# Kernel tuning notes

Measured on AMD Instinct MI355X. Metric: run time of the kernel, lower is better.

The kernel has to match this reference:

```python
import jax, jax.numpy as jnp
import numpy as np

C = 256
P = 8          # partition_size
DH = 32        # dim_head
NH = C // DH   # num heads
EXP = 4        # mlp expansion
EPS = 1e-5


def conv2d(x, w, b, stride, pad, groups):
    # x: NCHW, w: (O, I/groups, kh, kw)
    y = jax.lax.conv_general_dilated(
        x, w, (stride, stride), [(pad, pad), (pad, pad)],
        dimension_numbers=('NCHW', 'OIHW', 'NCHW'), feature_group_count=groups)
    return y + b[None, :, None, None]


def layernorm(x, g, b):
    m = jnp.mean(x, axis=-1, keepdims=True)
    v = jnp.mean((x - m) ** 2, axis=-1, keepdims=True)
    return (x - m) * jax.lax.rsqrt(v + EPS) * g + b


def partition_block(x):
    # (B,H,W,C) -> (B*nH*nW, P, P, C), MaxViT 'block' mode
    B, H, W, c = x.shape
    x = x.reshape(B, H // P, P, W // P, P, c)
    return x.transpose(0, 1, 3, 2, 4, 5).reshape(-1, P, P, c)


def reverse_block(w, H, W):
    c = w.shape[-1]
    x = w.reshape(-1, H // P, W // P, P, P, c)
    return x.transpose(0, 1, 3, 2, 4, 5).reshape(-1, H, W, c)


def window_attn(xw, qkv_w, qkv_b, proj_w, proj_b):
    # xw: (Nw, P, P, C); faithful to SelfAttentionCl (dropout inactive at eval)
    Nw = xw.shape[0]
    L = P * P
    qkv = xw.reshape(Nw, L, C) @ qkv_w.T + qkv_b           # (Nw, L, 3C)
    qkv = qkv.reshape(Nw, L, NH, 3 * DH).transpose(0, 2, 1, 3)  # (Nw, nh, L, 3dh)
    q, k, v = jnp.split(qkv, 3, axis=-1)
    attn = jax.nn.softmax((q @ jnp.swapaxes(k, -1, -2)) * (DH ** -0.5), axis=-1)
    o = (attn @ v).transpose(0, 2, 1, 3).reshape(Nw, P, P, C)
    return o @ proj_w.T + proj_b


def setup_inputs() -> dict:
    key = jax.random.key(0)
    ks = jax.random.split(key, 16)
    s = 0.02
    d = {
        'x': jax.random.normal(ks[0], (2, C, 256, 256), jnp.float32),
        'h': jnp.zeros((2, 256, 256, C), jnp.float32),
        'conv_w': s * jax.random.normal(ks[1], (C, 1, 3, 3), jnp.float32),
        'conv_b': jnp.zeros((C,), jnp.float32),
        'comb_w': s * jax.random.normal(ks[2], (C, 2, 7, 7), jnp.float32),
        'comb_b': jnp.zeros((C,), jnp.float32),
        'ln1_g': jnp.ones((C,), jnp.float32), 'ln1_b': jnp.zeros((C,), jnp.float32),
        'ln2_g': jnp.ones((C,), jnp.float32), 'ln2_b': jnp.zeros((C,), jnp.float32),
        'ln3_g': jnp.ones((C,), jnp.float32), 'ln3_b': jnp.zeros((C,), jnp.float32),
        'fsa_ln_g': jnp.ones((C,), jnp.float32), 'fsa_ln_b': jnp.zeros((C,), jnp.float32),
        'qkv_w': s * jax.random.normal(ks[3], (3 * C, C), jnp.float32),
        'qkv_b': jnp.zeros((3 * C,), jnp.float32),
        'proj_w': s * jax.random.normal(ks[4], (C, C), jnp.float32),
        'proj_b': jnp.zeros((C,), jnp.float32),
        'mlp_w1': s * jax.random.normal(ks[5], (EXP * C, C), jnp.float32),
        'mlp_b1': jnp.zeros((EXP * C,), jnp.float32),
        'mlp_w2': s * jax.random.normal(ks[6], (C, EXP * C), jnp.float32),
        'mlp_b2': jnp.zeros((C,), jnp.float32),
        'convg_w': s * jax.random.normal(ks[7], (C, 1, 7, 7), jnp.float32),
        'convg_b': jnp.zeros((C,), jnp.float32),
        'convh_w': s * jax.random.normal(ks[8], (C, 1, 7, 7), jnp.float32),
        'convh_b': jnp.zeros((C,), jnp.float32),
        'convf_w': s * jax.random.normal(ks[9], (C // 4, 4, 3, 3), jnp.float32),
        'convf_b': jnp.zeros((C // 4,), jnp.float32),
    }
    return d


def reference(x, h, conv_w, conv_b, comb_w, comb_b, ln1_g, ln1_b, ln2_g, ln2_b,
              ln3_g, ln3_b, fsa_ln_g, fsa_ln_b, qkv_w, qkv_b, proj_w, proj_b,
              mlp_w1, mlp_b1, mlp_w2, mlp_b2, convg_w, convg_b, convh_w, convh_b,
              convf_w, convf_b):
    relu = jax.nn.relu
    # depthwise conv + relu + LN (channels-last)
    x_conv = relu(conv2d(x, conv_w, conv_b, 1, 1, C)).transpose(0, 2, 3, 1)  # NHWC
    x_conv = layernorm(x_conv, ln1_g, ln1_b)
    H, W = x_conv.shape[1], x_conv.shape[2]
    # combine with recurrent state via grouped 7x7 conv (groups=C, 2 in-ch per group)
    xc = jnp.concatenate((x_conv, h), axis=3).transpose(0, 3, 1, 2)  # (B,2C,H,W)
    xc = conv2d(xc, comb_w, comb_b, 1, 3, C).transpose(0, 2, 3, 1)
    xc = layernorm(relu(xc), ln2_g, ln2_b)
    # block-windowed self-attention (UnifiedBlockGridAttention, mode='block')
    y = layernorm(xc, fsa_ln_g, fsa_ln_b)
    wins = partition_block(y)
    a = window_attn(wins, qkv_w, qkv_b, proj_w, proj_b)
    x_bsa = reverse_block(a, H, W)
    x_bsa = x_bsa + xc  # DropPath inactive (eval)
    x_bsa = layernorm(relu(x_bsa), ln3_g, ln3_b)
    # MLP (Linear -> GELU -> Linear), channels-last
    x_bsa = jax.nn.gelu(x_bsa @ mlp_w1.T + mlp_b1) @ mlp_w2.T + mlp_b2
    # output heads: depthwise 7x7 convs + grouped 3x3
    x_bsa = x_bsa.transpose(0, 3, 1, 2)
    x_bsa = relu(conv2d(x_bsa, convg_w, convg_b, 1, 3, C))
    h_new = relu(conv2d(x_bsa, convh_w, convh_b, 1, 3, C).transpose(0, 2, 3, 1))
    x_out = relu(conv2d(x_bsa, convf_w, convf_b, 1, 1, C // 4))
    return (x_out, h_new)
```

## Files before the change

kernel.cpp:

```cpp
#include <hip/hip_runtime.h>
#include <hip/hip_bf16.h>

#define HD 256
#define WD 256
#define CH 256
#define NB 2
#define NPIX (NB*HD*WD)

typedef __attribute__((ext_vector_type(4))) float f32x4;
typedef __attribute__((ext_vector_type(8))) short bf16x8;
typedef __attribute__((ext_vector_type(4))) short bf16x4;

__device__ __forceinline__ short f2bf(float f){
  unsigned u = __float_as_uint(f);
  u += 0x7fffu + ((u>>16)&1u);
  return (short)(u>>16);
}

__device__ __forceinline__ f32x4 mfma_bf16(bf16x8 a, bf16x8 b, f32x4 c){
  asm("v_mfma_f32_16x16x32_bf16 %0, %1, %2, %0" : "+v"(c) : "v"(a), "v"(b));
  return c;
}

__global__ __launch_bounds__(256) void k_cvtw(const float* __restrict__ qkvw,
    const float* __restrict__ projw, const float* __restrict__ w1,
    const float* __restrict__ w2, short* __restrict__ out){
  int i = blockIdx.x*256 + threadIdx.x;
  float v;
  if (i < 196608) v = qkvw[i];
  else if (i < 262144) v = projw[i-196608];
  else if (i < 524288) v = w1[i-262144];
  else v = w2[i-524288];
  out[i] = f2bf(v);
}

__global__ __launch_bounds__(256) void k_prepw(const float* __restrict__ combw,
    const float* __restrict__ gw, const float* __restrict__ hw,
    const float* __restrict__ fw, float* __restrict__ wT){
  int i = blockIdx.x*256 + threadIdx.x;
  if (i < 25088){
    int wi = i>>9, r = i&511, ii = r>>8, o = r&255;
    wT[i] = combw[o*98 + ii*49 + wi];
  } else if (i < 37632){
    int j = i-25088; int wi = j>>8, c = j&255;
    wT[i] = gw[c*49 + wi];
  } else if (i < 50176){
    int j = i-37632; int wi = j>>8, c = j&255;
    wT[i] = hw[c*49 + wi];
  } else if (i < 52480){
    int j = i-50176; int tap = j>>8, r = j&255, oc = r>>2, ic = r&3;
    wT[i] = fw[oc*36 + ic*9 + tap];
  }
}

__global__ __launch_bounds__(256) void k_conv3(const float* __restrict__ x,
    const float* __restrict__ w, const float* __restrict__ bias,
    const float* __restrict__ g1, const float* __restrict__ b1,
    float* __restrict__ out){
  int bid = blockIdx.x;
  int xb = bid & 15, y = (bid>>4) & 255, b = bid>>12;
  int t = threadIdx.x;
  __shared__ float tile[16][268];
  int xx0 = xb*16;
  {
    int xi = t & 15, cg = t >> 4;
    int xxg = xx0 + xi;
    #pragma unroll
    for (int k=0;k<16;++k){
      int c = cg*16 + k;
      const float* xp = x + ((size_t)(b*CH + c)*HD)*WD;
      float acc = bias[c];
      #pragma unroll
      for (int dy=-1; dy<=1; ++dy){
        int yy = y+dy;
        if ((unsigned)yy >= HD) continue;
        #pragma unroll
        for (int dx=-1; dx<=1; ++dx){
          int x2 = xxg+dx;
          if ((unsigned)x2 >= WD) continue;
          acc += xp[yy*WD + x2] * w[c*9 + (dy+1)*3 + (dx+1)];
        }
      }
      tile[xi][c] = fmaxf(acc, 0.f);
    }
  }
  __syncthreads();
  {
    int px = t >> 4, cs = t & 15;
    float4 m[4];
    #pragma unroll
    for (int j=0;j<4;++j) m[j] = *(const float4*)(&tile[px][cs*16 + j*4]);
    float s = 0.f, q = 0.f;
    #pragma unroll
    for (int j=0;j<4;++j){
      s += m[j].x+m[j].y+m[j].z+m[j].w;
      q += m[j].x*m[j].x+m[j].y*m[j].y+m[j].z*m[j].z+m[j].w*m[j].w;
    }
    #pragma unroll
    for (int o=1;o<16;o<<=1){ s += __shfl_xor(s,o); q += __shfl_xor(q,o); }
    float mean = s*(1.f/CH);
    float r = rsqrtf(q*(1.f/CH) - mean*mean + 1e-5f);
    size_t n = (size_t)(b*HD + y)*WD + xx0 + px;
    float* op = out + n*CH + cs*16;
    #pragma unroll
    for (int j=0;j<4;++j){
      float4 G = *(const float4*)(g1 + cs*16 + j*4);
      float4 Bb = *(const float4*)(b1 + cs*16 + j*4);
      float4 o4;
      o4.x = (m[j].x-mean)*r*G.x + Bb.x;
      o4.y = (m[j].y-mean)*r*G.y + Bb.y;
      o4.z = (m[j].z-mean)*r*G.z + Bb.z;
      o4.w = (m[j].w-mean)*r*G.w + Bb.w;
      *(float4*)(op + j*4) = o4;
    }
  }
}

__global__ __launch_bounds__(256) void k_comb(const float* __restrict__ xconv,
    const float* __restrict__ hbuf, const float* __restrict__ wT,
    const float* __restrict__ bias,
    const float* __restrict__ g2, const float* __restrict__ b2,
    const float* __restrict__ gf, const float* __restrict__ bfv,
    float* __restrict__ xc, short* __restrict__ ybuf){
  int bid = blockIdx.x;
  int xg = bid & 63, yb = (bid>>6) & 63, b = bid>>12;
  int wv = threadIdx.x>>6, lane = threadIdx.x & 63;
  int xx = xg*4 + wv, y0 = yb*4;
  const float* S = (lane < 32) ? xconv : hbuf;
  int cin = 8*(lane & 31);
  float4 bv = ((const float4*)bias)[lane];
  float4 acc[4];
  #pragma unroll
  for (int i=0;i<4;++i) acc[i] = bv;
  bool inty = (y0 >= 3) && (y0 <= HD-7);
  #pragma unroll 1
  for (int dx=0; dx<7; ++dx){
    int x2 = xx + dx - 3;
    bool vx = (unsigned)x2 < WD;
    float4 rA[10], rB[10];
    if (vx && inty){
      const float* base = S + ((size_t)((b*HD + y0-3)*WD + x2))*CH + cin;
      #pragma unroll
      for (int k=0;k<10;++k){
        const float4* p = (const float4*)(base + (size_t)k*WD*CH);
        rA[k] = p[0]; rB[k] = p[1];
      }
    } else {
      #pragma unroll
      for (int k=0;k<10;++k){
        int yy = y0 + k - 3;
        if (vx && (unsigned)yy < HD){
          const float4* p = (const float4*)(S + ((size_t)((b*HD+yy)*WD + x2))*CH + cin);
          rA[k] = p[0]; rB[k] = p[1];
        } else {
          rA[k] = float4{0,0,0,0}; rB[k] = float4{0,0,0,0};
        }
      }
    }
    #pragma unroll
    for (int dy=0; dy<7; ++dy){
      int wi = dy*7 + dx;
      float4 wa = ((const float4*)(wT + wi*512))[lane];
      float4 wb4 = ((const float4*)(wT + wi*512 + 256))[lane];
      #pragma unroll
      for (int yi=0; yi<4; ++yi){
        int k = yi + dy;
        acc[yi].x += rA[k].x*wa.x + rA[k].y*wb4.x;
        acc[yi].y += rA[k].z*wa.y + rA[k].w*wb4.y;
        acc[yi].z += rB[k].x*wa.z + rB[k].y*wb4.z;
        acc[yi].w += rB[k].z*wa.w + rB[k].w*wb4.w;
      }
    }
  }
  float4 G2 = ((const float4*)g2)[lane],  B2 = ((const float4*)b2)[lane];
  float4 GF = ((const float4*)gf)[lane],  BF = ((const float4*)bfv)[lane];
  #pragma unroll
  for (int yi=0; yi<4; ++yi){
    float4 v;
    v.x = fmaxf(acc[yi].x, 0.f); v.y = fmaxf(acc[yi].y, 0.f);
    v.z = fmaxf(acc[yi].z, 0.f); v.w = fmaxf(acc[yi].w, 0.f);
    float s = v.x+v.y+v.z+v.w;
    float q = v.x*v.x+v.y*v.y+v.z*v.z+v.w*v.w;
    #pragma unroll
    for (int o=1;o<64;o<<=1){ s += __shfl_xor(s,o); q += __shfl_xor(q,o); }
    float mean = s*(1.f/CH);
    float r = rsqrtf(q*(1.f/CH) - mean*mean + 1e-5f);
    float4 w4;
    w4.x = (v.x-mean)*r*G2.x + B2.x;
    w4.y = (v.y-mean)*r*G2.y + B2.y;
    w4.z = (v.z-mean)*r*G2.z + B2.z;
    w4.w = (v.w-mean)*r*G2.w + B2.w;
    size_t n = (size_t)((b*HD + y0+yi)*WD + xx);
    ((float4*)(xc + n*CH))[lane] = w4;
    float s2 = w4.x+w4.y+w4.z+w4.w;
    float q2 = w4.x*w4.x+w4.y*w4.y+w4.z*w4.z+w4.w*w4.w;
    #pragma unroll
    for (int o=1;o<64;o<<=1){ s2 += __shfl_xor(s2,o); q2 += __shfl_xor(q2,o); }
    float m2 = s2*(1.f/CH);
    float r2 = rsqrtf(q2*(1.f/CH) - m2*m2 + 1e-5f);
    bf16x4 yv;
    yv[0] = f2bf((w4.x-m2)*r2*GF.x + BF.x);
    yv[1] = f2bf((w4.y-m2)*r2*GF.y + BF.y);
    yv[2] = f2bf((w4.z-m2)*r2*GF.z + BF.z);
    yv[3] = f2bf((w4.w-m2)*r2*GF.w + BF.w);
    ((bf16x4*)(ybuf + n*CH))[lane] = yv;
  }
}

__global__ __launch_bounds__(256) void k_attn(const short* __restrict__ ybuf,
    const short* __restrict__ wqkv, const float* __restrict__ qkvb,
    const short* __restrict__ wproj, const float* __restrict__ pb,
    const float* __restrict__ xc, const float* __restrict__ g3,
    const float* __restrict__ b3, short* __restrict__ zbuf){
  __shared__ short wlds[24576];
  __shared__ short qs[64][40];
  __shared__ short ksm[64][40];
  __shared__ short vT[32][72];
  __shared__ short o2[2][64][36];
  __shared__ float redS[64][4];
  __shared__ float redQ[64][4];
  int wid = blockIdx.x;
  int b = wid>>10, wy = (wid>>5)&31, wx = wid&31;
  int t = threadIdx.x, wv = t>>6, lane = t&63;
  int g = lane>>4, c = lane&15;

  bf16x8 afr[8];
  {
    int tok = 16*wv + c;
    size_t n = (size_t)(b*HD + wy*8 + (tok>>3))*WD + wx*8 + (tok&7);
    const short* yp = ybuf + n*CH;
    #pragma unroll
    for (int ks=0;ks<8;++ks)
      afr[ks] = *(const bf16x8*)(yp + ks*32 + g*8);
  }
  {
    const short* wsrc = wqkv;
    #pragma unroll
    for (int i=0;i<12;++i){
      int rr = 24*wv + 2*i;
      int row = rr + (lane>>5);
      int colb = (lane&31)<<4;
      const short* gp = wsrc + row*256 + ((colb ^ ((row&7)<<4))>>1);
      __builtin_amdgcn_global_load_lds(
        (const __attribute__((address_space(1))) void*)gp,
        (__attribute__((address_space(3))) void*)(wlds + rr*256),
        16, 0, 0);
    }
  }
  __syncthreads();

  int s0 = c + 32*(g&1), s1 = s0 + 16;
  bool hiSel = (g & 2);

  f32x4 acc[4][4];
  #pragma unroll
  for (int mt=0;mt<4;++mt)
    #pragma unroll
    for (int nt=0;nt<4;++nt) acc[mt][nt] = (f32x4){0.f,0.f,0.f,0.f};

  #pragma unroll 1
  for (int hd=0; hd<8; ++hd){
    int cur = hd & 1;
    f32x4 qacc[6];
    #pragma unroll
    for (int nt=0;nt<6;++nt) qacc[nt] = (f32x4){0.f,0.f,0.f,0.f};
    #pragma unroll
    for (int nt=0; nt<6; ++nt){
      int R = nt*16 + c;
      const short* wr = wlds + R*256;
      int sw = (R&7)<<3;
      #pragma unroll
      for (int ks=0; ks<8; ++ks){
        bf16x8 bf = *(const bf16x8*)(wr + ((ks*32 + g*8) ^ sw));
        qacc[nt] = mfma_bf16(afr[ks], bf, qacc[nt]);
      }
    }
    #pragma unroll
    for (int nt=0; nt<6; ++nt){
      float bias = qkvb[hd*96 + nt*16 + c];
      if (nt<4){
        #pragma unroll
        for (int j=0;j<4;++j){
          short hv = f2bf(qacc[nt][j] + bias);
          int tok = 16*wv + 4*g + j;
          if (nt<2) qs[tok][nt*16 + c] = hv;
          else      ksm[tok][(nt-2)*16 + c] = hv;
        }
      } else {
        bf16x4 pk;
        #pragma unroll
        for (int j=0;j<4;++j) pk[j] = f2bf(qacc[nt][j] + bias);
        *(bf16x4*)(&vT[(nt-4)*16 + c][16*wv + 4*g]) = pk;
      }
    }
    __syncthreads();
    if (hd < 7){
      const short* wsrc = wqkv + (size_t)(hd+1)*24576;
      #pragma unroll
      for (int i=0;i<12;++i){
        int rr = 24*wv + 2*i;
        int row = rr + (lane>>5);
        int colb = (lane&31)<<4;
        const short* gp = wsrc + row*256 + ((colb ^ ((row&7)<<4))>>1);
        __builtin_amdgcn_global_load_lds(
          (const __attribute__((address_space(1))) void*)gp,
          (__attribute__((address_space(3))) void*)(wlds + rr*256),
          16, 0, 0);
      }
    }
    f32x4 sv[4];
    bf16x8 qa = *(const bf16x8*)(&qs[16*wv + c][g*8]);
    #pragma unroll
    for (int nt=0;nt<4;++nt){
      bf16x8 kb = *(const bf16x8*)(&ksm[nt*16 + c][g*8]);
      f32x4 z = (f32x4){0.f,0.f,0.f,0.f};
      sv[nt] = mfma_bf16(kb, qa, z);
    }
    float mx = sv[0][0];
    #pragma unroll
    for (int nt=0;nt<4;++nt)
      #pragma unroll
      for (int j=0;j<4;++j) mx = fmaxf(mx, sv[nt][j]);
    mx = fmaxf(mx, __shfl_xor(mx, 16));
    mx = fmaxf(mx, __shfl_xor(mx, 32));
    float sm = 0.f;
    #pragma unroll
    for (int nt=0;nt<4;++nt)
      #pragma unroll
      for (int j=0;j<4;++j){
        float e = __expf((sv[nt][j]-mx)*0.17677669529663687f);
        sv[nt][j] = e; sm += e;
      }
    sm += __shfl_xor(sm, 16);
    sm += __shfl_xor(sm, 32);
    float inv = 1.f/sm;
    unsigned pkLo[4], pkHi[4];
    #pragma unroll
    for (int nt=0;nt<4;++nt){
      pkLo[nt] = (unsigned)(unsigned short)f2bf(sv[nt][0]) | ((unsigned)(unsigned short)f2bf(sv[nt][1])<<16);
      pkHi[nt] = (unsigned)(unsigned short)f2bf(sv[nt][2]) | ((unsigned)(unsigned short)f2bf(sv[nt][3])<<16);
    }
    bf16x8 pa[2];
    #pragma unroll
    for (int k2=0;k2<2;++k2){
      int n0 = 2*k2, n1 = 2*k2+1;
      unsigned w0a = __shfl((int)pkLo[n0], s0), w0b = __shfl((int)pkLo[n1], s0);
      unsigned w1a = __shfl((int)pkHi[n0], s0), w1b = __shfl((int)pkHi[n1], s0);
      unsigned w2a = __shfl((int)pkLo[n0], s1), w2b = __shfl((int)pkLo[n1], s1);
      unsigned w3a = __shfl((int)pkHi[n0], s1), w3b = __shfl((int)pkHi[n1], s1);
      union { unsigned u[4]; bf16x8 v; } U;
      U.u[0] = hiSel ? w0b : w0a;
      U.u[1] = hiSel ? w1b : w1a;
      U.u[2] = hiSel ? w2b : w2a;
      U.u[3] = hiSel ? w3b : w3a;
      pa[k2] = U.v;
    }
    f32x4 ov[2];
    ov[0] = (f32x4){0.f,0.f,0.f,0.f}; ov[1] = (f32x4){0.f,0.f,0.f,0.f};
    #pragma unroll
    for (int k2=0;k2<2;++k2){
      #pragma unroll
      for (int nt=0;nt<2;++nt){
        bf16x8 vb = *(const bf16x8*)(&vT[nt*16 + c][k2*32 + g*8]);
        ov[nt] = mfma_bf16(pa[k2], vb, ov[nt]);
      }
    }
    #pragma unroll
    for (int j=0;j<4;++j){
      float invO = __shfl(inv, 4*g + j);
      int tok = 16*wv + 4*g + j;
      o2[cur][tok][c]      = f2bf(ov[0][j]*invO);
      o2[cur][tok][16 + c] = f2bf(ov[1][j]*invO);
    }
    __syncthreads();
    #pragma unroll
    for (int mt=0;mt<4;++mt){
      bf16x8 a = *(const bf16x8*)(&o2[cur][mt*16+c][g*8]);
      #pragma unroll
      for (int nt=0;nt<4;++nt){
        bf16x8 bfr = *(const bf16x8*)(wproj + (size_t)(wv*64 + nt*16 + c)*256 + hd*32 + g*8);
        acc[mt][nt] = mfma_bf16(a, bfr, acc[mt][nt]);
      }
    }
  }
  #pragma unroll
  for (int mt=0;mt<4;++mt){
    #pragma unroll
    for (int j=0;j<4;++j){
      int row_l = mt*16 + 4*g + j;
      size_t n = (size_t)(b*HD + wy*8 + (row_l>>3))*WD + wx*8 + (row_l&7);
      float ps_ = 0.f, pq_ = 0.f;
      #pragma unroll
      for (int nt=0;nt<4;++nt){
        int col = wv*64 + nt*16 + c;
        float v = acc[mt][nt][j] + pb[col] + xc[n*CH + col];
        v = fmaxf(v, 0.f);
        acc[mt][nt][j] = v;
        ps_ += v; pq_ += v*v;
      }
      #pragma unroll
      for (int o=1;o<16;o<<=1){ ps_ += __shfl_xor(ps_,o); pq_ += __shfl_xor(pq_,o); }
      if (c==0){ redS[row_l][wv] = ps_; redQ[row_l][wv] = pq_; }
    }
  }
  __syncthreads();
  #pragma unroll
  for (int mt=0;mt<4;++mt){
    #pragma unroll
    for (int j=0;j<4;++j){
      int row_l = mt*16 + 4*g + j;
      size_t n = (size_t)(b*HD + wy*8 + (row_l>>3))*WD + wx*8 + (row_l&7);
      float st = redS[row_l][0]+redS[row_l][1]+redS[row_l][2]+redS[row_l][3];
      float qt = redQ[row_l][0]+redQ[row_l][1]+redQ[row_l][2]+redQ[row_l][3];
      float mean = st*(1.f/CH);
      float rs = rsqrtf(qt*(1.f/CH) - mean*mean + 1e-5f);
      #pragma unroll
      for (int nt=0;nt<4;++nt){
        int col = wv*64 + nt*16 + c;
        float y = (acc[mt][nt][j]-mean)*rs*g3[col] + b3[col];
        zbuf[n*CH + col] = f2bf(y);
      }
    }
  }
}

__global__ __launch_bounds__(256) void k_mlp(const short* __restrict__ zbuf,
    const short* __restrict__ w1, const short* __restrict__ w2,
    const float* __restrict__ b1, const float* __restrict__ b2,
    float* __restrict__ bsa){
  __shared__ short zt[64][264];
  __shared__ short hid[64][136];
  int blk = blockIdx.x, t = threadIdx.x;
  int wv=t>>6, lane=t&63, g=lane>>4, c=lane&15;
  size_t m0 = (size_t)blk*64;
  {
    int row=t>>2, seg=t&3;
    const uint4* s = (const uint4*)(zbuf + (m0+row)*CH + seg*64);
    uint4* d = (uint4*)(&zt[row][seg*64]);
    #pragma unroll
    for (int i=0;i<8;++i) d[i] = s[i];
  }
  __syncthreads();
  f32x4 acc2[4][4];
  #pragma unroll
  for (int mt=0;mt<4;++mt)
    #pragma unroll
    for (int nt=0;nt<4;++nt) acc2[mt][nt] = (f32x4){0.f,0.f,0.f,0.f};
  #pragma unroll 1
  for (int hc=0; hc<8; ++hc){
    f32x4 a1[4][2];
    #pragma unroll
    for (int mt=0;mt<4;++mt){ a1[mt][0]=(f32x4){0.f,0.f,0.f,0.f}; a1[mt][1]=(f32x4){0.f,0.f,0.f,0.f}; }
    #pragma unroll 1
    for (int ks=0;ks<8;++ks){
      bf16x8 a[4];
      #pragma unroll
      for (int mt=0;mt<4;++mt) a[mt] = *(const bf16x8*)(&zt[mt*16+c][ks*32+g*8]);
      #pragma unroll
      for (int nl=0;nl<2;++nl){
        int o = hc*128 + (wv*2+nl)*16 + c;
        bf16x8 bfr = *(const bf16x8*)(w1 + (size_t)o*256 + ks*32 + g*8);
        #pragma unroll
        for (int mt=0;mt<4;++mt)
          a1[mt][nl] = mfma_bf16(a[mt], bfr, a1[mt][nl]);
      }
    }
    __syncthreads();
    #pragma unroll
    for (int mt=0;mt<4;++mt)
      #pragma unroll
      for (int nl=0;nl<2;++nl){
        int ol = (wv*2+nl)*16 + c;
        float bias = b1[hc*128 + ol];
        #pragma unroll
        for (int j=0;j<4;++j){
          float v = a1[mt][nl][j] + bias;
          float u = 0.7978845608f*(v + 0.044715f*v*v*v);
          float e = __expf(-2.f*fabsf(u));
          float th = (1.f-e)/(1.f+e);
          th = (u>=0.f)? th : -th;
          v = 0.5f*v*(1.f+th);
          hid[mt*16 + 4*g + j][ol] = f2bf(v);
        }
      }
    __syncthreads();
    #pragma unroll 1
    for (int k2=0;k2<4;++k2){
      bf16x8 a[4];
      #pragma unroll
      for (int mt=0;mt<4;++mt) a[mt] = *(const bf16x8*)(&hid[mt*16+c][k2*32+g*8]);
      #pragma unroll
      for (int nt=0;nt<4;++nt){
        bf16x8 bfr = *(const bf16x8*)(w2 + (size_t)(wv*64+nt*16+c)*1024 + hc*128 + k2*32 + g*8);
        #pragma unroll
        for (int mt=0;mt<4;++mt)
          acc2[mt][nt] = mfma_bf16(a[mt], bfr, acc2[mt][nt]);
      }
    }
    __syncthreads();
  }
  #pragma unroll
  for (int mt=0;mt<4;++mt)
    #pragma unroll
    for (int nt=0;nt<4;++nt){
      int col = wv*64 + nt*16 + c;
      #pragma unroll
      for (int j=0;j<4;++j){
        int row_l = mt*16 + 4*g + j;
        bsa[(m0+row_l)*CH + col] = acc2[mt][nt][j] + b2[col];
      }
    }
}

__global__ __launch_bounds__(256) void k_dw7(const float* __restrict__ src,
    const float* __restrict__ wT, const float* __restrict__ bias, float* __restrict__ dst){
  int bid = blockIdx.x;
  int xg = bid & 63, yb = (bid>>6) & 31, b = bid>>11;
  int wv = threadIdx.x>>6, lane = threadIdx.x & 63;
  int xx = xg*4 + wv, y0 = yb*8;
  float4 bv = ((const float4*)bias)[lane];
  float4 acc[8];
  #pragma unroll
  for (int i=0;i<8;++i) acc[i] = bv;
  bool inty = (y0 >= 3) && (y0 <= HD-11);
  #pragma unroll 1
  for (int dx=0; dx<7; ++dx){
    int x2 = xx + dx - 3;
    bool vx = (unsigned)x2 < WD;
    float4 r[14];
    if (vx && inty){
      const float* base = src + ((size_t)((b*HD + y0-3)*WD + x2))*CH;
      #pragma unroll
      for (int k=0;k<14;++k)
        r[k] = ((const float4*)(base + (size_t)k*WD*CH))[lane];
    } else {
      #pragma unroll
      for (int k=0;k<14;++k){
        int yy = y0 + k - 3;
        if (vx && (unsigned)yy < HD)
          r[k] = ((const float4*)(src + ((size_t)((b*HD+yy)*WD + x2))*CH))[lane];
        else r[k] = float4{0,0,0,0};
      }
    }
    #pragma unroll
    for (int dy=0; dy<7; ++dy){
      int wi = dy*7 + dx;
      float4 wv4 = ((const float4*)(wT + wi*256))[lane];
      #pragma unroll
      for (int yi=0; yi<8; ++yi){
        acc[yi].x += r[yi+dy].x * wv4.x;
        acc[yi].y += r[yi+dy].y * wv4.y;
        acc[yi].z += r[yi+dy].z * wv4.z;
        acc[yi].w += r[yi+dy].w * wv4.w;
      }
    }
  }
  #pragma unroll
  for (int yi=0; yi<8; ++yi){
    float4 o;
    o.x = fmaxf(acc[yi].x, 0.f); o.y = fmaxf(acc[yi].y, 0.f);
    o.z = fmaxf(acc[yi].z, 0.f); o.w = fmaxf(acc[yi].w, 0.f);
    ((float4*)(dst + ((size_t)((b*HD+y0+yi)*WD + xx))*CH))[lane] = o;
  }
}

__global__ __launch_bounds__(256) void k_convf(const float* __restrict__ gsrc,
    const float* __restrict__ wTf, const float* __restrict__ bias, float* __restrict__ out){
  __shared__ float ot[4][8][65];
  int bid = blockIdx.x;
  int xg = bid & 63, yb = (bid>>6) & 31, b = bid>>11;
  int wv = threadIdx.x>>6, lane = threadIdx.x & 63;
  int xx = xg*4 + wv, y0 = yb*8;
  float bv = bias[lane];
  float acc[8];
  #pragma unroll
  for (int i=0;i<8;++i) acc[i] = 0.f;
  bool inty = (y0 >= 1) && (y0 <= HD-9);
  #pragma unroll 1
  for (int dx=0; dx<3; ++dx){
    int x2 = xx + dx - 1;
    bool vx = (unsigned)x2 < WD;
    float4 r[10];
    if (vx && inty){
      const float* base = gsrc + ((size_t)((b*HD + y0-1)*WD + x2))*CH;
      #pragma unroll
      for (int k=0;k<10;++k)
        r[k] = ((const float4*)(base + (size_t)k*WD*CH))[lane];
    } else {
      #pragma unroll
      for (int k=0;k<10;++k){
        int yy = y0 + k - 1;
        if (vx && (unsigned)yy < HD)
          r[k] = ((const float4*)(gsrc + ((size_t)((b*HD+yy)*WD + x2))*CH))[lane];
        else r[k] = float4{0,0,0,0};
      }
    }
    #pragma unroll
    for (int dy=0; dy<3; ++dy){
      float4 w4 = ((const float4*)(wTf + (dy*3+dx)*256))[lane];
      #pragma unroll
      for (int yi=0; yi<8; ++yi)
        acc[yi] += r[yi+dy].x*w4.x + r[yi+dy].y*w4.y + r[yi+dy].z*w4.z + r[yi+dy].w*w4.w;
    }
  }
  #pragma unroll
  for (int yi=0; yi<8; ++yi) ot[wv][yi][lane] = fmaxf(acc[yi] + bv, 0.f);
  __syncthreads();
  #pragma unroll
  for (int rep=0; rep<2; ++rep){
    int p = rep*256 + threadIdx.x;
    int oc = p>>3, yi = p&7;
    float4 v;
    v.x = ot[0][yi][oc]; v.y = ot[1][yi][oc]; v.z = ot[2][yi][oc]; v.w = ot[3][yi][oc];
    *(float4*)(out + (((size_t)(b*64+oc))*HD + y0+yi)*WD + xg*4) = v;
  }
}

extern "C" void kernel_launch(void* const* d_in, const int* in_sizes, int n_in,
                              void* d_out, int out_size, void* d_ws, size_t ws_size,
                              hipStream_t stream) {
  const float* x      = (const float*)d_in[0];
  const float* hbuf   = (const float*)d_in[1];
  const float* conv_w = (const float*)d_in[2];
  const float* conv_b = (const float*)d_in[3];
  const float* comb_w = (const float*)d_in[4];
  const float* comb_b = (const float*)d_in[5];
  const float* ln1_g  = (const float*)d_in[6];
  const float* ln1_b  = (const float*)d_in[7];
  const float* ln2_g  = (const float*)d_in[8];
  const float* ln2_b  = (const float*)d_in[9];
  const float* ln3_g  = (const float*)d_in[10];
  const float* ln3_b  = (const float*)d_in[11];
  const float* fsa_g  = (const float*)d_in[12];
  const float* fsa_b  = (const float*)d_in[13];
  const float* qkv_w  = (const float*)d_in[14];
  const float* qkv_b  = (const float*)d_in[15];
  const float* proj_w = (const float*)d_in[16];
  const float* proj_b = (const float*)d_in[17];
  const float* mlp_w1 = (const float*)d_in[18];
  const float* mlp_b1 = (const float*)d_in[19];
  const float* mlp_w2 = (const float*)d_in[20];
  const float* mlp_b2 = (const float*)d_in[21];
  const float* convg_w= (const float*)d_in[22];
  const float* convg_b= (const float*)d_in[23];
  const float* convh_w= (const float*)d_in[24];
  const float* convh_b= (const float*)d_in[25];
  const float* convf_w= (const float*)d_in[26];
  const float* convf_b= (const float*)d_in[27];
  float* out = (float*)d_out;
  char* ws = (char*)d_ws;

  float* xconv = (float*)(ws);
  short* zbuf  = (short*)(ws + 67108864);
  float* xc    = (float*)(ws + 134217728);
  float* bsa   = (float*)(ws + 134217728);
  short* ybuf  = (short*)(ws + 268435456);
  float* gbuf  = (float*)(ws + 335544320);
  short* wb    = (short*)(ws + 469762048);
  float* wT    = (float*)(ws + 471334912);

  k_cvtw<<<3072,256,0,stream>>>(qkv_w, proj_w, mlp_w1, mlp_w2, wb);
  k_prepw<<<205,256,0,stream>>>(comb_w, convg_w, convh_w, convf_w, wT);
  k_conv3<<<8192,256,0,stream>>>(x, conv_w, conv_b, ln1_g, ln1_b, xconv);
  k_comb<<<8192,256,0,stream>>>(xconv, hbuf, wT, comb_b, ln2_g, ln2_b, fsa_g, fsa_b, xc, ybuf);
  k_attn<<<2048,256,0,stream>>>(ybuf, wb, qkv_b, wb+196608, proj_b, xc, ln3_g, ln3_b, zbuf);
  k_mlp<<<2048,256,0,stream>>>(zbuf, wb+262144, wb+524288, mlp_b1, mlp_b2, bsa);
  k_dw7<<<4096,256,0,stream>>>(bsa, wT+25088, convg_b, gbuf);
  k_dw7<<<4096,256,0,stream>>>(gbuf, wT+37632, convh_b, out + 8388608);
  k_convf<<<4096,256,0,stream>>>(gbuf, wT+50176, convf_b, out);
}
```

Before: 1.409 ms.

## Store conv/comb intermediates in fp16 and use packed fdot2 in grouped 7x7 conv

The 3x3 conv output, the recurrent state h (converted by a new kernel), and the combined-conv output xc are now stored as fp16 instead of fp32. The grouped 7x7 combine conv reads these half-width buffers and computes with v_dot2 fp16 instructions against fp16-packed weights. This halves the memory traffic of the bandwidth-heavy comb kernel and of the xc residual read in attention. In exchange it adds an extra pass to convert h and loses precision in the intermediates and the residual path.

```diff
diff --git a/kernel.cpp b/kernel.cpp
--- a/kernel.cpp
+++ b/kernel.cpp
@@ -10,6 +10,9 @@
 typedef __attribute__((ext_vector_type(4))) float f32x4;
 typedef __attribute__((ext_vector_type(8))) short bf16x8;
 typedef __attribute__((ext_vector_type(4))) short bf16x4;
+typedef __fp16 f16x2 __attribute__((ext_vector_type(2)));
+
+union U16 { uint4 q; f16x2 h[4]; };
 
 __device__ __forceinline__ short f2bf(float f){
   unsigned u = __float_as_uint(f);
@@ -32,6 +35,18 @@
   else if (i < 524288) v = w1[i-262144];
   else v = w2[i-524288];
   out[i] = f2bf(v);
+}
+
+__global__ __launch_bounds__(256) void k_cvth(const float* __restrict__ h, short* __restrict__ hh){
+  int i = blockIdx.x*256 + threadIdx.x;
+  const float4* p = ((const float4*)h) + (size_t)i*2;
+  float4 a = p[0], b4 = p[1];
+  U16 W;
+  W.h[0] = __builtin_amdgcn_cvt_pkrtz(a.x, a.y);
+  W.h[1] = __builtin_amdgcn_cvt_pkrtz(a.z, a.w);
+  W.h[2] = __builtin_amdgcn_cvt_pkrtz(b4.x, b4.y);
+  W.h[3] = __builtin_amdgcn_cvt_pkrtz(b4.z, b4.w);
+  ((uint4*)hh)[i] = W.q;
 }
 
 __global__ __launch_bounds__(256) void k_prepw(const float* __restrict__ combw,
@@ -50,13 +65,18 @@
   } else if (i < 52480){
     int j = i-50176; int tap = j>>8, r = j&255, oc = r>>2, ic = r&3;
     wT[i] = fw[oc*36 + ic*9 + tap];
+  } else {
+    int j = i-52480;
+    int wi = j>>9, r2 = j&511;
+    int o = r2>>1, ii = r2&1;
+    ((__fp16*)wT)[104960 + j] = (__fp16)combw[o*98 + ii*49 + wi];
   }
 }
 
 __global__ __launch_bounds__(256) void k_conv3(const float* __restrict__ x,
     const float* __restrict__ w, const float* __restrict__ bias,
     const float* __restrict__ g1, const float* __restrict__ b1,
-    float* __restrict__ out){
+    short* __restrict__ out){
   int bid = blockIdx.x;
   int xb = bid & 15, y = (bid>>4) & 255, b = bid>>12;
   int t = threadIdx.x;
@@ -101,7 +121,8 @@
     float mean = s*(1.f/CH);
     float r = rsqrtf(q*(1.f/CH) - mean*mean + 1e-5f);
     size_t n = (size_t)(b*HD + y)*WD + xx0 + px;
-    float* op = out + n*CH + cs*16;
+    short* op = out + n*CH + cs*16;
+    U16 W0, W1;
     #pragma unroll
     for (int j=0;j<4;++j){
       float4 G = *(const float4*)(g1 + cs*16 + j*4);
@@ -111,22 +132,27 @@
       o4.y = (m[j].y-mean)*r*G.y + Bb.y;
       o4.z = (m[j].z-mean)*r*G.z + Bb.z;
       o4.w = (m[j].w-mean)*r*G.w + Bb.w;
-      *(float4*)(op + j*4) = o4;
-    }
-  }
-}
-
-__global__ __launch_bounds__(256) void k_comb(const float* __restrict__ xconv,
-    const float* __restrict__ hbuf, const float* __restrict__ wT,
+      f16x2 p0 = __builtin_amdgcn_cvt_pkrtz(o4.x, o4.y);
+      f16x2 p1 = __builtin_amdgcn_cvt_pkrtz(o4.z, o4.w);
+      if (j<2){ W0.h[2*j] = p0; W0.h[2*j+1] = p1; }
+      else    { W1.h[2*(j-2)] = p0; W1.h[2*(j-2)+1] = p1; }
+    }
+    *(uint4*)op = W0.q;
+    *(uint4*)(op+8) = W1.q;
+  }
+}
+
+__global__ __launch_bounds__(256) void k_comb(const short* __restrict__ xcv,
+    const short* __restrict__ hh, const short* __restrict__ wTh,
     const float* __restrict__ bias,
     const float* __restrict__ g2, const float* __restrict__ b2,
     const float* __restrict__ gf, const float* __restrict__ bfv,
-    float* __restrict__ xc, short* __restrict__ ybuf){
+    short* __restrict__ xch, short* __restrict__ ybuf){
   int bid = blockIdx.x;
   int xg = bid & 63, yb = (bid>>6) & 63, b = bid>>12;
   int wv = threadIdx.x>>6, lane = threadIdx.x & 63;
   int xx = xg*4 + wv, y0 = yb*4;
-  const float* S = (lane < 32) ? xconv : hbuf;
+  const short* S = (lane < 32) ? xcv : hh;
   int cin = 8*(lane & 31);
   float4 bv = ((const float4*)bias)[lane];
   float4 acc[4];
@@ -137,38 +163,32 @@
   for (int dx=0; dx<7; ++dx){
     int x2 = xx + dx - 3;
     bool vx = (unsigned)x2 < WD;
-    float4 rA[10], rB[10];
+    uint4 r[10];
     if (vx && inty){
-      const float* base = S + ((size_t)((b*HD + y0-3)*WD + x2))*CH + cin;
-      #pragma unroll
-      for (int k=0;k<10;++k){
-        const float4* p = (const float4*)(base + (size_t)k*WD*CH);
-        rA[k] = p[0]; rB[k] = p[1];
-      }
+      const short* base = S + ((size_t)((b*HD + y0-3)*WD + x2))*CH + cin;
+      #pragma unroll
+      for (int k=0;k<10;++k)
+        r[k] = *(const uint4*)(base + (size_t)k*WD*CH);
     } else {
       #pragma unroll
       for (int k=0;k<10;++k){
         int yy = y0 + k - 3;
-        if (vx && (unsigned)yy < HD){
-          const float4* p = (const float4*)(S + ((size_t)((b*HD+yy)*WD + x2))*CH + cin);
-          rA[k] = p[0]; rB[k] = p[1];
-        } else {
-          rA[k] = float4{0,0,0,0}; rB[k] = float4{0,0,0,0};
-        }
+        if (vx && (unsigned)yy < HD)
+          r[k] = *(const uint4*)(S + ((size_t)((b*HD+yy)*WD + x2))*CH + cin);
+        else r[k] = uint4{0,0,0,0};
       }
     }
     #pragma unroll
     for (int dy=0; dy<7; ++dy){
       int wi = dy*7 + dx;
-      float4 wa = ((const float4*)(wT + wi*512))[lane];
-      float4 wb4 = ((const float4*)(wT + wi*512 + 256))[lane];
+      U16 wq; wq.q = ((const uint4*)wTh)[wi*64 + lane];
       #pragma unroll
       for (int yi=0; yi<4; ++yi){
-        int k = yi + dy;
-        acc[yi].x += rA[k].x*wa.x + rA[k].y*wb4.x;
-        acc[yi].y += rA[k].z*wa.y + rA[k].w*wb4.y;
-        acc[yi].z += rB[k].x*wa.z + rB[k].y*wb4.z;
-        acc[yi].w += rB[k].z*wa.w + rB[k].w*wb4.w;
+        U16 d; d.q = r[yi+dy];
+        acc[yi].x = __builtin_amdgcn_fdot2(d.h[0], wq.h[0], acc[yi].x, false);
+        acc[yi].y = __builtin_amdgcn_fdot2(d.h[1], wq.h[1], acc[yi].y, false);
+        acc[yi].z = __builtin_amdgcn_fdot2(d.h[2], wq.h[2], acc[yi].z, false);
+        acc[yi].w = __builtin_amdgcn_fdot2(d.h[3], wq.h[3], acc[yi].w, false);
       }
     }
   }
@@ -191,7 +211,10 @@
     w4.z = (v.z-mean)*r*G2.z + B2.z;
     w4.w = (v.w-mean)*r*G2.w + B2.w;
     size_t n = (size_t)((b*HD + y0+yi)*WD + xx);
-    ((float4*)(xc + n*CH))[lane] = w4;
+    union { f16x2 h[2]; uint2 u; } P;
+    P.h[0] = __builtin_amdgcn_cvt_pkrtz(w4.x, w4.y);
+    P.h[1] = __builtin_amdgcn_cvt_pkrtz(w4.z, w4.w);
+    *(uint2*)(xch + n*CH + 4*lane) = P.u;
     float s2 = w4.x+w4.y+w4.z+w4.w;
     float q2 = w4.x*w4.x+w4.y*w4.y+w4.z*w4.z+w4.w*w4.w;
     #pragma unroll
@@ -210,7 +233,7 @@
 __global__ __launch_bounds__(256) void k_attn(const short* __restrict__ ybuf,
     const short* __restrict__ wqkv, const float* __restrict__ qkvb,
     const short* __restrict__ wproj, const float* __restrict__ pb,
-    const float* __restrict__ xc, const float* __restrict__ g3,
+    const __fp16* __restrict__ xc, const float* __restrict__ g3,
     const float* __restrict__ b3, short* __restrict__ zbuf){
   __shared__ short wlds[24576];
   __shared__ short qs[64][40];
@@ -393,7 +416,7 @@
       #pragma unroll
       for (int nt=0;nt<4;++nt){
         int col = wv*64 + nt*16 + c;
-        float v = acc[mt][nt][j] + pb[col] + xc[n*CH + col];
+        float v = acc[mt][nt][j] + pb[col] + (float)xc[n*CH + col];
         v = fmaxf(v, 0.f);
         acc[mt][nt][j] = v;
         ps_ += v; pq_ += v*v;
@@ -650,20 +673,23 @@
   float* out = (float*)d_out;
   char* ws = (char*)d_ws;
 
-  float* xconv = (float*)(ws);
-  short* zbuf  = (short*)(ws + 67108864);
-  float* xc    = (float*)(ws + 134217728);
-  float* bsa   = (float*)(ws + 134217728);
-  short* ybuf  = (short*)(ws + 268435456);
-  float* gbuf  = (float*)(ws + 335544320);
-  short* wb    = (short*)(ws + 469762048);
-  float* wT    = (float*)(ws + 471334912);
+  short* xcv  = (short*)(ws);
+  short* hh   = (short*)(ws + 67108864);
+  short* zbuf = (short*)(ws + 67108864);
+  short* xch  = (short*)(ws + 134217728);
+  float* bsa  = (float*)(ws + 134217728);
+  short* ybuf = (short*)(ws + 268435456);
+  float* gbuf = (float*)(ws + 335544320);
+  short* wb   = (short*)(ws + 469762048);
+  float* wT   = (float*)(ws + 471334912);
+  short* wTh  = (short*)wT + 104960;
 
   k_cvtw<<<3072,256,0,stream>>>(qkv_w, proj_w, mlp_w1, mlp_w2, wb);
-  k_prepw<<<205,256,0,stream>>>(comb_w, convg_w, convh_w, convf_w, wT);
-  k_conv3<<<8192,256,0,stream>>>(x, conv_w, conv_b, ln1_g, ln1_b, xconv);
-  k_comb<<<8192,256,0,stream>>>(xconv, hbuf, wT, comb_b, ln2_g, ln2_b, fsa_g, fsa_b, xc, ybuf);
-  k_attn<<<2048,256,0,stream>>>(ybuf, wb, qkv_b, wb+196608, proj_b, xc, ln3_g, ln3_b, zbuf);
+  k_prepw<<<303,256,0,stream>>>(comb_w, convg_w, convh_w, convf_w, wT);
+  k_cvth<<<16384,256,0,stream>>>(hbuf, hh);
+  k_conv3<<<8192,256,0,stream>>>(x, conv_w, conv_b, ln1_g, ln1_b, xcv);
+  k_comb<<<8192,256,0,stream>>>(xcv, hh, wTh, comb_b, ln2_g, ln2_b, fsa_g, fsa_b, xch, ybuf);
+  k_attn<<<2048,256,0,stream>>>(ybuf, wb, qkv_b, wb+196608, proj_b, (const __fp16*)xch, ln3_g, ln3_b, zbuf);
   k_mlp<<<2048,256,0,stream>>>(zbuf, wb+262144, wb+524288, mlp_b1, mlp_b2, bsa);
   k_dw7<<<4096,256,0,stream>>>(bsa, wT+25088, convg_b, gbuf);
   k_dw7<<<4096,256,0,stream>>>(gbuf, wT+37632, convh_b, out + 8388608);
```

After: 1.244 ms. 11.7% less time.
